# Kernel tuning notes

Hardware: AMD Instinct MI355X
Metric: run time of the kernel (lower is better)

## Reference

```python
import jax, jax.numpy as jnp
import numpy as np

NUM_HEADS = 8  # matches init_kwargs

def setup_inputs() -> dict:
    key = jax.random.key(0)
    ks = jax.random.split(key, 5)
    b, n, c = 8, 4096, 512
    scale_in = 1.0 / np.sqrt(c)
    return {
        'x': jax.random.normal(ks[0], (b, n, c), jnp.float32),
        'wqkv_w': jax.random.normal(ks[1], (3 * c, c), jnp.float32) * scale_in,
        'wqkv_b': jax.random.normal(ks[2], (3 * c,), jnp.float32) * 0.02,
        'wp_w': jax.random.normal(ks[3], (c, c), jnp.float32) * scale_in,
        'wp_b': jax.random.normal(ks[4], (c,), jnp.float32) * 0.02,
    }

def reference(x, wqkv_w, wqkv_b, wp_w, wp_b):
    b, n, c = x.shape
    h = NUM_HEADS
    d = c // h
    # QKV projection (torch Linear: x @ W^T + b)
    qkv = x @ wqkv_w.T + wqkv_b                      # (b, n, 3c)
    qkv = jnp.transpose(qkv.reshape(b, n, 3, c), (2, 0, 1, 3))
    q, k, v = qkv[0], qkv[1], qkv[2]                 # each (b, n, c)
    # Faithful to original: reshape (b,n,h,d) -> (b,h,n,d) is a FLAT
    # reinterpretation (torch .reshape), not a transpose.
    q = q.reshape(b, n, h, d).reshape(b, h, n, d)
    k = k.reshape(b, n, h, d).reshape(b, h, n, d)
    v = v.reshape(b, n, h, d).reshape(b, h, n, d)
    # Channel (cross-covariance) attention: contract over tokens n.
    scores = jnp.einsum('bhnd,bhne->bhde', q, k) / jnp.sqrt(jnp.float32(d))
    weights = jax.nn.softmax(scores, axis=-1)        # softmax over head_dim
    y = jnp.einsum('bhde,bhme->bhdm', weights, v)    # (b, h, d, n)
    y = jnp.transpose(y, (0, 3, 1, 2)).reshape(b, n, c)
    return y @ wp_w.T + wp_b
```

## Files before the change

### kernel.cpp

```cpp
#include <hip/hip_runtime.h>

typedef short s16x8 __attribute__((ext_vector_type(8)));
typedef float f32x4 __attribute__((ext_vector_type(4)));
typedef unsigned short us;

__device__ inline us f2bf(float f){
    union{float f;unsigned u;} v{f};
    unsigned r = v.u + 0x7fff + ((v.u>>16)&1);
    return (us)(r>>16);
}

__device__ __forceinline__ void glds16(const us* g, us* l){
    __builtin_amdgcn_global_load_lds(
        (const __attribute__((address_space(1))) unsigned int*)(g),
        (__attribute__((address_space(3))) unsigned int*)(l), 16, 0, 0);
}

__global__ void cast_x(const float* __restrict__ src, us* __restrict__ dst, int n4){
    int i = blockIdx.x*blockDim.x + threadIdx.x;
    if(i < n4){
        float4 f = ((const float4*)src)[i];
        ushort4 o;
        o.x = f2bf(f.x); o.y = f2bf(f.y); o.z = f2bf(f.z); o.w = f2bf(f.w);
        ((ushort4*)dst)[i] = o;
    }
}

__global__ void cast_w(const float* __restrict__ wqkv_w, const float* __restrict__ wp_w,
                       us* __restrict__ wqkvbf, us* __restrict__ wpbf){
    int i = blockIdx.x*blockDim.x + threadIdx.x;
    const float* s; us* d; int j;
    if(i < 196608){ s = wqkv_w; d = wqkvbf; j = i; }
    else          { s = wp_w;   d = wpbf;   j = i - 196608; }
    float4 f = ((const float4*)s)[j];
    ushort4 o;
    o.x = f2bf(f.x); o.y = f2bf(f.y); o.z = f2bf(f.z); o.w = f2bf(f.w);
    ((ushort4*)d)[j] = o;
}

__launch_bounds__(256,2)
__global__ void gemm_qkv(const us* __restrict__ A, const us* __restrict__ B,
                         const float* __restrict__ bias, us* __restrict__ C){
    __shared__ __attribute__((aligned(16))) us sA[128*32];
    __shared__ __attribute__((aligned(16))) us sB[128*32];
    int t = threadIdx.x;
    int id = blockIdx.x;
    int xcd = id & 7, s = id >> 3;
    int nt = s % 12, mt = xcd*32 + s/12;
    int lane = t&63, wave = t>>6, quad = lane>>4, l15 = lane&15;
    int wm = wave>>1, wn = wave&1;

    int srow = wave*32 + (lane>>2);
    int scol = (lane&3)*8;
    const us* Ag = A + (size_t)(mt*128 + srow)*512 + scol;
    const us* Bg = B + (size_t)(nt*128 + srow)*512 + scol;
    us* sAw = &sA[(wave*32)*32];
    us* sBw = &sB[(wave*32)*32];

    f32x4 acc[4][4];
    #pragma unroll
    for(int i=0;i<4;i++)
        #pragma unroll
        for(int j=0;j<4;j++) acc[i][j] = (f32x4){0.f,0.f,0.f,0.f};

    for(int k0=0; k0<512; k0+=32){
        glds16(Ag + k0,          sAw);
        glds16(Ag + 16*512 + k0, sAw + 16*32);
        glds16(Bg + k0,          sBw);
        glds16(Bg + 16*512 + k0, sBw + 16*32);
        __syncthreads();
        s16x8 af[4], bfr[4];
        #pragma unroll
        for(int i=0;i<4;i++) af[i]  = *(const s16x8*)&sA[(wm*64 + i*16 + l15)*32 + quad*8];
        #pragma unroll
        for(int j=0;j<4;j++) bfr[j] = *(const s16x8*)&sB[(wn*64 + j*16 + l15)*32 + quad*8];
        #pragma unroll
        for(int i=0;i<4;i++)
            #pragma unroll
            for(int j=0;j<4;j++)
                acc[i][j] = __builtin_amdgcn_mfma_f32_16x16x32_bf16(af[i], bfr[j], acc[i][j], 0,0,0);
        __syncthreads();
    }

    int row0 = mt*128 + wm*64, col0 = nt*128 + wn*64;
    #pragma unroll
    for(int j=0;j<4;j++){
        int col = col0 + j*16 + l15;
        float bv = bias[col];
        #pragma unroll
        for(int i=0;i<4;i++){
            int rbase = row0 + i*16 + quad*4;
            #pragma unroll
            for(int r=0;r<4;r++)
                C[(size_t)(rbase+r)*1536 + col] = f2bf(acc[i][j][r] + bv);
        }
    }
}

__launch_bounds__(256,4)
__global__ void attn_scores_mfma(const us* __restrict__ qkv, float* __restrict__ Sp){
    __shared__ __attribute__((aligned(16))) us sQt[64*72];
    __shared__ __attribute__((aligned(16))) us sKt[64*72];
    int t = threadIdx.x;
    int kb = blockIdx.x, head = blockIdx.y;
    int lane = t & 63, w = t >> 6;
    int quad = lane >> 4, l15 = lane & 15;
    int p = t & 31;
    int d0 = (t >> 5) * 8;

    f32x4 acc[4];
    #pragma unroll
    for(int j=0;j<4;j++) acc[j] = (f32x4){0.f,0.f,0.f,0.f};

    for(int chunk=0; chunk<8; chunk++){
        int r0 = head*512 + kb*64 + chunk*8;
        const us* g = qkv + (size_t)(r0 + (p>>2))*1536 + (2*(p&3))*64 + d0;
        union{uint4 v; us h[8];} q0, q1, k0, k1;
        q0.v = *(const uint4*)g;         q1.v = *(const uint4*)(g + 64);
        k0.v = *(const uint4*)(g + 512); k1.v = *(const uint4*)(g + 576);
        #pragma unroll
        for(int j=0;j<8;j++){
            *(unsigned*)&sQt[(d0+j)*72 + 2*p] = (unsigned)q0.h[j] | ((unsigned)q1.h[j]<<16);
            *(unsigned*)&sKt[(d0+j)*72 + 2*p] = (unsigned)k0.h[j] | ((unsigned)k1.h[j]<<16);
        }
        __syncthreads();
        int d = w*16 + l15;
        #pragma unroll
        for(int ks=0; ks<2; ks++){
            int tb = ks*4 + quad;
            s16x8 af = *(const s16x8*)&sQt[d*72 + tb*8];
            #pragma unroll
            for(int jt=0; jt<4; jt++){
                int e = jt*16 + l15;
                s16x8 bfv = *(const s16x8*)&sKt[e*72 + tb*8];
                acc[jt] = __builtin_amdgcn_mfma_f32_16x16x32_bf16(af, bfv, acc[jt], 0,0,0);
            }
        }
        __syncthreads();
    }

    float* S = Sp + (size_t)(kb*64 + head)*4096;
    #pragma unroll
    for(int jt=0; jt<4; jt++){
        int e = jt*16 + l15;
        #pragma unroll
        for(int r=0; r<4; r++){
            int d = w*16 + quad*4 + r;
            S[d*64 + e] = acc[jt][r];
        }
    }
}

__launch_bounds__(256,1)
__global__ void smfold(const float* __restrict__ Sp, const us* __restrict__ wpbf,
                       us* __restrict__ Mcat){
    __shared__ us sWt[64*72];
    int t = threadIdx.x;
    int head = blockIdx.x, b = head>>3, h = head&7;
    int lane = t&63, w = t>>6, quad = lane>>4, l15 = lane&15;

    {
        int d = t>>2, eg = (t&3)*16;
        float v[16];
        #pragma unroll
        for(int e=0;e<16;e++) v[e]=0.f;
        for(int kb=0; kb<8; kb++){
            const float* pp = Sp + (size_t)(kb*64 + head)*4096 + d*64 + eg;
            #pragma unroll
            for(int e4=0;e4<4;e4++){
                float4 f = ((const float4*)pp)[e4];
                v[e4*4+0]+=f.x; v[e4*4+1]+=f.y; v[e4*4+2]+=f.z; v[e4*4+3]+=f.w;
            }
        }
        float m = -1e30f;
        #pragma unroll
        for(int e=0;e<16;e++){ v[e] *= 0.125f; m = fmaxf(m, v[e]); }
        m = fmaxf(m, __shfl_xor(m, 1));
        m = fmaxf(m, __shfl_xor(m, 2));
        float s = 0.f;
        #pragma unroll
        for(int e=0;e<16;e++){ v[e] = __expf(v[e]-m); s += v[e]; }
        s += __shfl_xor(s, 1);
        s += __shfl_xor(s, 2);
        float inv = 1.f/s;
        #pragma unroll
        for(int e=0;e<16;e++) sWt[(eg+e)*72 + d] = f2bf(v[e]*inv);
    }
    __syncthreads();

    #pragma unroll
    for(int i=0;i<8;i++){
        int nO = w*128 + i*16 + l15;
        s16x8 af0 = *(const s16x8*)&wpbf[(size_t)nO*512 + h*64 + quad*8];
        s16x8 af1 = *(const s16x8*)&wpbf[(size_t)nO*512 + h*64 + 32 + quad*8];
        #pragma unroll
        for(int j=0;j<4;j++){
            s16x8 bf0 = *(const s16x8*)&sWt[(j*16+l15)*72 + quad*8];
            s16x8 bf1 = *(const s16x8*)&sWt[(j*16+l15)*72 + 32 + quad*8];
            f32x4 acc = (f32x4){0.f,0.f,0.f,0.f};
            acc = __builtin_amdgcn_mfma_f32_16x16x32_bf16(af0, bf0, acc, 0,0,0);
            acc = __builtin_amdgcn_mfma_f32_16x16x32_bf16(af1, bf1, acc, 0,0,0);
            #pragma unroll
            for(int r=0;r<4;r++){
                int row = w*128 + i*16 + quad*4 + r;
                Mcat[((size_t)(b*512 + row))*512 + h*64 + j*16 + l15] = f2bf(acc[r]);
            }
        }
    }
}

__launch_bounds__(256,2)
__global__ void gemm_vout(const us* __restrict__ qkv, const us* __restrict__ Mcat,
                          const float* __restrict__ bias, float* __restrict__ out){
    __shared__ __attribute__((aligned(16))) us sA[128*32];
    __shared__ __attribute__((aligned(16))) us sB[128*32];
    int t = threadIdx.x;
    int id = blockIdx.x;
    int xcd = id & 7, s = id >> 3;
    int nt = s & 3, mt = xcd*32 + (s>>2);
    int b = mt>>5, mr = mt&31;
    int lane = t&63, wave = t>>6, quad = lane>>4, l15 = lane&15;
    int wm = wave>>1, wn = wave&1;

    int r = wave*32 + (lane>>2);
    int m = mr*128 + r;
    const us* Abase = qkv + ((size_t)(8*b)*512 + (m>>3))*1536 + 1024 + (m&7)*64 + (lane&3)*8;
    us* sAw = &sA[(wave*32)*32];

    int srB = wave*32 + (lane>>2), scB = (lane&3)*8;
    const us* Bg = Mcat + ((size_t)(b*512 + nt*128 + srB))*512 + scB;
    us* sBw = &sB[(wave*32)*32];

    f32x4 acc[4][4];
    #pragma unroll
    for(int i=0;i<4;i++)
        #pragma unroll
        for(int j=0;j<4;j++) acc[i][j] = (f32x4){0.f,0.f,0.f,0.f};

    for(int ki=0; ki<16; ki++){
        int k0 = ki*32;
        int h = k0>>6, e0 = k0&63;
        const us* Ag = Abase + (size_t)h*512*1536 + e0;
        glds16(Ag,            sAw);
        glds16(Ag + 2*1536,   sAw + 16*32);
        glds16(Bg + k0,           sBw);
        glds16(Bg + 16*512 + k0,  sBw + 16*32);
        __syncthreads();
        s16x8 af[4], bfr[4];
        #pragma unroll
        for(int i=0;i<4;i++) af[i]  = *(const s16x8*)&sA[(wm*64 + i*16 + l15)*32 + quad*8];
        #pragma unroll
        for(int j=0;j<4;j++) bfr[j] = *(const s16x8*)&sB[(wn*64 + j*16 + l15)*32 + quad*8];
        #pragma unroll
        for(int i=0;i<4;i++)
            #pragma unroll
            for(int j=0;j<4;j++)
                acc[i][j] = __builtin_amdgcn_mfma_f32_16x16x32_bf16(af[i], bfr[j], acc[i][j], 0,0,0);
        __syncthreads();
    }

    int row0 = b*4096 + mr*128 + wm*64;
    int col0 = nt*128 + wn*64;
    #pragma unroll
    for(int j=0;j<4;j++){
        int col = col0 + j*16 + l15;
        float bv = bias[col];
        #pragma unroll
        for(int i=0;i<4;i++){
            int rbase = row0 + i*16 + quad*4;
            #pragma unroll
            for(int r2=0;r2<4;r2++)
                out[(size_t)(rbase+r2)*512 + col] = acc[i][j][r2] + bv;
        }
    }
}

extern "C" void kernel_launch(void* const* d_in, const int* in_sizes, int n_in,
                              void* d_out, int out_size, void* d_ws, size_t ws_size,
                              hipStream_t stream){
    const float* x      = (const float*)d_in[0];
    const float* wqkv_w = (const float*)d_in[1];
    const float* wqkv_b = (const float*)d_in[2];
    const float* wp_w   = (const float*)d_in[3];
    const float* wp_b   = (const float*)d_in[4];

    char* ws = (char*)d_ws;
    us*    qkvbf  = (us*)(ws);
    us*    xbf    = (us*)(ws + 100663296);
    float* Spart  = (float*)(ws + 134217728);
    us*    Mcat   = (us*)(ws + 142606336);
    us*    wqkvbf = (us*)(ws + 146800640);
    us*    wpbf   = (us*)(ws + 148373504);

    cast_w<<<1024,256,0,stream>>>(wqkv_w, wp_w, wqkvbf, wpbf);
    cast_x<<<16384,256,0,stream>>>(x, xbf, 16777216/4);

    gemm_qkv<<<3072,256,0,stream>>>(xbf, wqkvbf, wqkv_b, qkvbf);

    attn_scores_mfma<<<dim3(8,64),256,0,stream>>>(qkvbf, Spart);

    smfold<<<64,256,0,stream>>>(Spart, wpbf, Mcat);

    gemm_vout<<<1024,256,0,stream>>>(qkvbf, Mcat, wp_b, (float*)d_out);
}
```

Before: 252.3 us.

## Deepen GEMM K-tiles with swizzled LDS, split scores more, separate softmax and fold

Both GEMMs now stage 64-wide K tiles in LDS with an XOR swizzle. This halves the number of barrier iterations and is meant to avoid LDS bank conflicts on the fragment reads. The scores kernel uses 16 token blocks instead of 8 to get more parallelism. The softmax+fold kernel is split into a standalone softmax kernel and a fold kernel spread over 4x more blocks. The changes add an extra launch, a Wsm buffer round-trip, more partial-sum traffic and larger shared memory per block.

```diff
diff --git a/kernel.cpp b/kernel.cpp
--- a/kernel.cpp
+++ b/kernel.cpp
@@ -41,8 +41,8 @@
 __launch_bounds__(256,2)
 __global__ void gemm_qkv(const us* __restrict__ A, const us* __restrict__ B,
                          const float* __restrict__ bias, us* __restrict__ C){
-    __shared__ __attribute__((aligned(16))) us sA[128*32];
-    __shared__ __attribute__((aligned(16))) us sB[128*32];
+    __shared__ __attribute__((aligned(16))) us sA[128*64];
+    __shared__ __attribute__((aligned(16))) us sB[128*64];
     int t = threadIdx.x;
     int id = blockIdx.x;
     int xcd = id & 7, s = id >> 3;
@@ -50,12 +50,12 @@
     int lane = t&63, wave = t>>6, quad = lane>>4, l15 = lane&15;
     int wm = wave>>1, wn = wave&1;
 
-    int srow = wave*32 + (lane>>2);
-    int scol = (lane&3)*8;
-    const us* Ag = A + (size_t)(mt*128 + srow)*512 + scol;
-    const us* Bg = B + (size_t)(nt*128 + srow)*512 + scol;
-    us* sAw = &sA[(wave*32)*32];
-    us* sBw = &sB[(wave*32)*32];
+    int l8 = lane>>3;
+    int sw = ((lane&7) ^ l8)*8;
+    const us* Ag = A + (size_t)(mt*128 + wave*32 + l8)*512 + sw;
+    const us* Bg = B + (size_t)(nt*128 + wave*32 + l8)*512 + sw;
+    us* sAw = &sA[(wave*32)*64];
+    us* sBw = &sB[(wave*32)*64];
 
     f32x4 acc[4][4];
     #pragma unroll
@@ -63,22 +63,36 @@
         #pragma unroll
         for(int j=0;j<4;j++) acc[i][j] = (f32x4){0.f,0.f,0.f,0.f};
 
-    for(int k0=0; k0<512; k0+=32){
-        glds16(Ag + k0,          sAw);
-        glds16(Ag + 16*512 + k0, sAw + 16*32);
-        glds16(Bg + k0,          sBw);
-        glds16(Bg + 16*512 + k0, sBw + 16*32);
-        __syncthreads();
-        s16x8 af[4], bfr[4];
-        #pragma unroll
-        for(int i=0;i<4;i++) af[i]  = *(const s16x8*)&sA[(wm*64 + i*16 + l15)*32 + quad*8];
-        #pragma unroll
-        for(int j=0;j<4;j++) bfr[j] = *(const s16x8*)&sB[(wn*64 + j*16 + l15)*32 + quad*8];
-        #pragma unroll
-        for(int i=0;i<4;i++)
-            #pragma unroll
-            for(int j=0;j<4;j++)
-                acc[i][j] = __builtin_amdgcn_mfma_f32_16x16x32_bf16(af[i], bfr[j], acc[i][j], 0,0,0);
+    for(int k0=0; k0<512; k0+=64){
+        glds16(Ag + k0,           sAw);
+        glds16(Ag + 8*512 + k0,   sAw + 8*64);
+        glds16(Ag + 16*512 + k0,  sAw + 16*64);
+        glds16(Ag + 24*512 + k0,  sAw + 24*64);
+        glds16(Bg + k0,           sBw);
+        glds16(Bg + 8*512 + k0,   sBw + 8*64);
+        glds16(Bg + 16*512 + k0,  sBw + 16*64);
+        glds16(Bg + 24*512 + k0,  sBw + 24*64);
+        __syncthreads();
+        #pragma unroll
+        for(int ks=0; ks<2; ks++){
+            int kc = ks*4 + quad;
+            s16x8 af[4], bfr[4];
+            #pragma unroll
+            for(int i=0;i<4;i++){
+                int r = wm*64 + i*16 + l15;
+                af[i] = *(const s16x8*)&sA[r*64 + ((kc ^ (r&7))<<3)];
+            }
+            #pragma unroll
+            for(int j=0;j<4;j++){
+                int r = wn*64 + j*16 + l15;
+                bfr[j] = *(const s16x8*)&sB[r*64 + ((kc ^ (r&7))<<3)];
+            }
+            #pragma unroll
+            for(int i=0;i<4;i++)
+                #pragma unroll
+                for(int j=0;j<4;j++)
+                    acc[i][j] = __builtin_amdgcn_mfma_f32_16x16x32_bf16(af[i], bfr[j], acc[i][j], 0,0,0);
+        }
         __syncthreads();
     }
 
@@ -112,8 +126,8 @@
     #pragma unroll
     for(int j=0;j<4;j++) acc[j] = (f32x4){0.f,0.f,0.f,0.f};
 
-    for(int chunk=0; chunk<8; chunk++){
-        int r0 = head*512 + kb*64 + chunk*8;
+    for(int chunk=0; chunk<4; chunk++){
+        int r0 = head*512 + kb*32 + chunk*8;
         const us* g = qkv + (size_t)(r0 + (p>>2))*1536 + (2*(p&3))*64 + d0;
         union{uint4 v; us h[8];} q0, q1, k0, k1;
         q0.v = *(const uint4*)g;         q1.v = *(const uint4*)(g + 64);
@@ -151,46 +165,60 @@
     }
 }
 
-__launch_bounds__(256,1)
-__global__ void smfold(const float* __restrict__ Sp, const us* __restrict__ wpbf,
-                       us* __restrict__ Mcat){
+__global__ void softmax64(const float* __restrict__ Sp, us* __restrict__ W){
+    int head = blockIdx.x;
+    int t = threadIdx.x;
+    int d = t>>2, eg = (t&3)*16;
+    float v[16];
+    #pragma unroll
+    for(int e=0;e<16;e++) v[e]=0.f;
+    for(int kb=0; kb<16; kb++){
+        const float* pp = Sp + (size_t)(kb*64 + head)*4096 + d*64 + eg;
+        #pragma unroll
+        for(int e4=0;e4<4;e4++){
+            float4 f = ((const float4*)pp)[e4];
+            v[e4*4+0]+=f.x; v[e4*4+1]+=f.y; v[e4*4+2]+=f.z; v[e4*4+3]+=f.w;
+        }
+    }
+    float m = -1e30f;
+    #pragma unroll
+    for(int e=0;e<16;e++){ v[e] *= 0.125f; m = fmaxf(m, v[e]); }
+    m = fmaxf(m, __shfl_xor(m, 1));
+    m = fmaxf(m, __shfl_xor(m, 2));
+    float s = 0.f;
+    #pragma unroll
+    for(int e=0;e<16;e++){ v[e] = __expf(v[e]-m); s += v[e]; }
+    s += __shfl_xor(s, 1);
+    s += __shfl_xor(s, 2);
+    float inv = 1.f/s;
+    union{uint4 u[2]; us h[16];} o;
+    #pragma unroll
+    for(int e=0;e<16;e++) o.h[e] = f2bf(v[e]*inv);
+    uint4* wp = (uint4*)(W + (size_t)head*4096 + d*64 + eg);
+    wp[0] = o.u[0]; wp[1] = o.u[1];
+}
+
+__launch_bounds__(256,2)
+__global__ void fold(const us* __restrict__ Wsm, const us* __restrict__ wpbf,
+                     us* __restrict__ Mcat){
     __shared__ us sWt[64*72];
     int t = threadIdx.x;
-    int head = blockIdx.x, b = head>>3, h = head&7;
+    int head = blockIdx.x>>2, part = blockIdx.x&3;
+    int b = head>>3, h = head&7;
     int lane = t&63, w = t>>6, quad = lane>>4, l15 = lane&15;
-
-    {
-        int d = t>>2, eg = (t&3)*16;
-        float v[16];
-        #pragma unroll
-        for(int e=0;e<16;e++) v[e]=0.f;
-        for(int kb=0; kb<8; kb++){
-            const float* pp = Sp + (size_t)(kb*64 + head)*4096 + d*64 + eg;
-            #pragma unroll
-            for(int e4=0;e4<4;e4++){
-                float4 f = ((const float4*)pp)[e4];
-                v[e4*4+0]+=f.x; v[e4*4+1]+=f.y; v[e4*4+2]+=f.z; v[e4*4+3]+=f.w;
-            }
-        }
-        float m = -1e30f;
-        #pragma unroll
-        for(int e=0;e<16;e++){ v[e] *= 0.125f; m = fmaxf(m, v[e]); }
-        m = fmaxf(m, __shfl_xor(m, 1));
-        m = fmaxf(m, __shfl_xor(m, 2));
-        float s = 0.f;
-        #pragma unroll
-        for(int e=0;e<16;e++){ v[e] = __expf(v[e]-m); s += v[e]; }
-        s += __shfl_xor(s, 1);
-        s += __shfl_xor(s, 2);
-        float inv = 1.f/s;
-        #pragma unroll
-        for(int e=0;e<16;e++) sWt[(eg+e)*72 + d] = f2bf(v[e]*inv);
+    #pragma unroll
+    for(int it=0; it<2; it++){
+        int idx = it*2048 + t*8;
+        int d = idx>>6, e0 = idx&63;
+        union{uint4 v; us s[8];} q;
+        q.v = *(const uint4*)&Wsm[(size_t)head*4096 + idx];
+        #pragma unroll
+        for(int j=0;j<8;j++) sWt[(e0+j)*72 + d] = q.s[j];
     }
     __syncthreads();
-
-    #pragma unroll
-    for(int i=0;i<8;i++){
-        int nO = w*128 + i*16 + l15;
+    #pragma unroll
+    for(int i=0;i<2;i++){
+        int nO = part*128 + w*32 + i*16 + l15;
         s16x8 af0 = *(const s16x8*)&wpbf[(size_t)nO*512 + h*64 + quad*8];
         s16x8 af1 = *(const s16x8*)&wpbf[(size_t)nO*512 + h*64 + 32 + quad*8];
         #pragma unroll
@@ -202,7 +230,7 @@
             acc = __builtin_amdgcn_mfma_f32_16x16x32_bf16(af1, bf1, acc, 0,0,0);
             #pragma unroll
             for(int r=0;r<4;r++){
-                int row = w*128 + i*16 + quad*4 + r;
+                int row = part*128 + w*32 + i*16 + quad*4 + r;
                 Mcat[((size_t)(b*512 + row))*512 + h*64 + j*16 + l15] = f2bf(acc[r]);
             }
         }
@@ -212,8 +240,8 @@
 __launch_bounds__(256,2)
 __global__ void gemm_vout(const us* __restrict__ qkv, const us* __restrict__ Mcat,
                           const float* __restrict__ bias, float* __restrict__ out){
-    __shared__ __attribute__((aligned(16))) us sA[128*32];
-    __shared__ __attribute__((aligned(16))) us sB[128*32];
+    __shared__ __attribute__((aligned(16))) us sA[128*64];
+    __shared__ __attribute__((aligned(16))) us sB[128*64];
     int t = threadIdx.x;
     int id = blockIdx.x;
     int xcd = id & 7, s = id >> 3;
@@ -222,14 +250,12 @@
     int lane = t&63, wave = t>>6, quad = lane>>4, l15 = lane&15;
     int wm = wave>>1, wn = wave&1;
 
-    int r = wave*32 + (lane>>2);
-    int m = mr*128 + r;
-    const us* Abase = qkv + ((size_t)(8*b)*512 + (m>>3))*1536 + 1024 + (m&7)*64 + (lane&3)*8;
-    us* sAw = &sA[(wave*32)*32];
-
-    int srB = wave*32 + (lane>>2), scB = (lane&3)*8;
-    const us* Bg = Mcat + ((size_t)(b*512 + nt*128 + srB))*512 + scB;
-    us* sBw = &sB[(wave*32)*32];
+    int l8 = lane>>3;
+    int sw = ((lane&7) ^ l8)*8;
+    const us* Abase = qkv + ((size_t)(8*b)*512 + mr*16 + wave*4)*1536 + 1024 + l8*64 + sw;
+    const us* Bbase = Mcat + ((size_t)(b*512 + nt*128 + wave*32 + l8))*512 + sw;
+    us* sAw = &sA[(wave*32)*64];
+    us* sBw = &sB[(wave*32)*64];
 
     f32x4 acc[4][4];
     #pragma unroll
@@ -237,25 +263,38 @@
         #pragma unroll
         for(int j=0;j<4;j++) acc[i][j] = (f32x4){0.f,0.f,0.f,0.f};
 
-    for(int ki=0; ki<16; ki++){
-        int k0 = ki*32;
-        int h = k0>>6, e0 = k0&63;
-        const us* Ag = Abase + (size_t)h*512*1536 + e0;
-        glds16(Ag,            sAw);
-        glds16(Ag + 2*1536,   sAw + 16*32);
-        glds16(Bg + k0,           sBw);
-        glds16(Bg + 16*512 + k0,  sBw + 16*32);
-        __syncthreads();
-        s16x8 af[4], bfr[4];
-        #pragma unroll
-        for(int i=0;i<4;i++) af[i]  = *(const s16x8*)&sA[(wm*64 + i*16 + l15)*32 + quad*8];
-        #pragma unroll
-        for(int j=0;j<4;j++) bfr[j] = *(const s16x8*)&sB[(wn*64 + j*16 + l15)*32 + quad*8];
-        #pragma unroll
-        for(int i=0;i<4;i++)
-            #pragma unroll
-            for(int j=0;j<4;j++)
-                acc[i][j] = __builtin_amdgcn_mfma_f32_16x16x32_bf16(af[i], bfr[j], acc[i][j], 0,0,0);
+    for(int h=0; h<8; h++){
+        const us* Ah = Abase + (size_t)h*512*1536;
+        const us* Bh = Bbase + h*64;
+        glds16(Ah,           sAw);
+        glds16(Ah + 1536,    sAw + 8*64);
+        glds16(Ah + 2*1536,  sAw + 16*64);
+        glds16(Ah + 3*1536,  sAw + 24*64);
+        glds16(Bh,           sBw);
+        glds16(Bh + 8*512,   sBw + 8*64);
+        glds16(Bh + 16*512,  sBw + 16*64);
+        glds16(Bh + 24*512,  sBw + 24*64);
+        __syncthreads();
+        #pragma unroll
+        for(int ks=0; ks<2; ks++){
+            int kc = ks*4 + quad;
+            s16x8 af[4], bfr[4];
+            #pragma unroll
+            for(int i=0;i<4;i++){
+                int r = wm*64 + i*16 + l15;
+                af[i] = *(const s16x8*)&sA[r*64 + ((kc ^ (r&7))<<3)];
+            }
+            #pragma unroll
+            for(int j=0;j<4;j++){
+                int r = wn*64 + j*16 + l15;
+                bfr[j] = *(const s16x8*)&sB[r*64 + ((kc ^ (r&7))<<3)];
+            }
+            #pragma unroll
+            for(int i=0;i<4;i++)
+                #pragma unroll
+                for(int j=0;j<4;j++)
+                    acc[i][j] = __builtin_amdgcn_mfma_f32_16x16x32_bf16(af[i], bfr[j], acc[i][j], 0,0,0);
+        }
         __syncthreads();
     }
 
@@ -288,18 +327,19 @@
     us*    qkvbf  = (us*)(ws);
     us*    xbf    = (us*)(ws + 100663296);
     float* Spart  = (float*)(ws + 134217728);
-    us*    Mcat   = (us*)(ws + 142606336);
-    us*    wqkvbf = (us*)(ws + 146800640);
-    us*    wpbf   = (us*)(ws + 148373504);
+    us*    Wsm    = (us*)(ws + 150994944);
+    us*    Mcat   = (us*)(ws + 151519232);
+    us*    wqkvbf = (us*)(ws + 155713536);
+    us*    wpbf   = (us*)(ws + 157286400);
 
     cast_w<<<1024,256,0,stream>>>(wqkv_w, wp_w, wqkvbf, wpbf);
     cast_x<<<16384,256,0,stream>>>(x, xbf, 16777216/4);
 
     gemm_qkv<<<3072,256,0,stream>>>(xbf, wqkvbf, wqkv_b, qkvbf);
 
-    attn_scores_mfma<<<dim3(8,64),256,0,stream>>>(qkvbf, Spart);
-
-    smfold<<<64,256,0,stream>>>(Spart, wpbf, Mcat);
+    attn_scores_mfma<<<dim3(16,64),256,0,stream>>>(qkvbf, Spart);
+    softmax64<<<64,256,0,stream>>>(Spart, Wsm);
+    fold<<<256,256,0,stream>>>(Wsm, wpbf, Mcat);
 
     gemm_vout<<<1024,256,0,stream>>>(qkvbf, Mcat, wp_b, (float*)d_out);
 }
```

After: 234.4 us. 1.08x faster.
